# Optimization experiments

Measured on AMD Instinct MI355X. Metric: run time of the kernel, lower is better.

The kernel has to match this reference:

```python
import jax, jax.numpy as jnp
import numpy as np

E = 1024
H = 16
DH = E // H
LN_EPS = 1e-5


def setup_inputs() -> dict:
    key = jax.random.key(0)
    ks = jax.random.split(key, 9)
    B, Lq, Lk = 8, 1024, 1024
    s = 0.02
    return {
        "query": jax.random.normal(ks[0], (B, Lq, E), jnp.float32),
        "key_t": jax.random.normal(ks[1], (B, Lk, E), jnp.float32),
        "value": jax.random.normal(ks[2], (B, Lk, E), jnp.float32),
        "in_proj_w": jax.random.normal(ks[3], (3 * E, E), jnp.float32) * s,
        "in_proj_b": jnp.zeros((3 * E,), jnp.float32),
        "out_proj_w": jax.random.normal(ks[4], (E, E), jnp.float32) * s,
        "out_proj_b": jnp.zeros((E,), jnp.float32),
        "ln_gamma": jnp.ones((E,), jnp.float32),
        "ln_beta": jnp.zeros((E,), jnp.float32),
    }


def _mha_cross(query, key_t, value, in_proj_w, in_proj_b, out_proj_w, out_proj_b,
               ln_gamma, ln_beta):
    B, Lq, _ = query.shape
    Lk = key_t.shape[1]
    wq, wk, wv = in_proj_w[:E], in_proj_w[E:2 * E], in_proj_w[2 * E:]
    bq, bk, bv = in_proj_b[:E], in_proj_b[E:2 * E], in_proj_b[2 * E:]
    # projections (torch Linear: x @ W^T + b)
    q = (query @ wq.T + bq).reshape(B, Lq, H, DH)
    k = (key_t @ wk.T + bk).reshape(B, Lk, H, DH)
    v = (value @ wv.T + bv).reshape(B, Lk, H, DH)
    scale = 1.0 / np.sqrt(DH).astype(np.float32)
    # unfused attention: explicit [B,H,Lq,Lk] scores (need_weights=True path)
    scores = jnp.einsum("bqhd,bkhd->bhqk", q, k) * scale
    probs = jax.nn.softmax(scores, axis=-1)
    attn = jnp.einsum("bhqk,bkhd->bqhd", probs, v).reshape(B, Lq, E)
    attn_out = attn @ out_proj_w.T + out_proj_b
    # averaged attention weights (average_attn_weights=True default)
    attn_weights = probs.mean(axis=1)  # [B, Lq, Lk]
    # residual + LayerNorm
    x = query + attn_out
    mu = x.mean(axis=-1, keepdims=True)
    var = x.var(axis=-1, keepdims=True)
    y = (x - mu) * jax.lax.rsqrt(var + LN_EPS) * ln_gamma + ln_beta
    return y, attn_weights


def reference(query, key_t, value, in_proj_w, in_proj_b, out_proj_w, out_proj_b,
              ln_gamma, ln_beta):
    return _mha_cross(query, key_t, value, in_proj_w, in_proj_b,
                      out_proj_w, out_proj_b, ln_gamma, ln_beta)
```

## Files before the change

kernel.cpp:

```cpp
#include <hip/hip_runtime.h>
#include <stdint.h>

#define E_DIM 1024
#define H_NUM 16
#define B_NUM 8
#define LQ 1024
#define LK 1024
#define MROWS (B_NUM * LQ)

typedef unsigned short u16;
typedef __attribute__((ext_vector_type(8))) short bf16x8;
typedef __attribute__((ext_vector_type(4))) short bf16x4;
typedef __attribute__((ext_vector_type(4))) float f32x4;
typedef bf16x8 __attribute__((may_alias)) bf16x8_ma;
typedef bf16x4 __attribute__((may_alias)) bf16x4_ma;
typedef f32x4 __attribute__((may_alias)) f32x4_ma;

typedef __attribute__((address_space(1))) const void* gas_ptr;
typedef __attribute__((address_space(3))) void* las_ptr;

__device__ __forceinline__ void gload16(const void* g, void* l) {
  __builtin_amdgcn_global_load_lds((gas_ptr)g, (las_ptr)l, 16, 0, 0);
}

__device__ __forceinline__ u16 f2bf(float f) {
  union { float f; uint32_t u; } c; c.f = f;
  return (u16)((c.u + 0x7FFFu + ((c.u >> 16) & 1u)) >> 16);
}

#define MFMA_BF16(a, b, c) __builtin_amdgcn_mfma_f32_16x16x32_bf16((a), (b), (c), 0, 0, 0)

#define SCALE_Q 0.18033688011112042f

__global__ __launch_bounds__(256) void cvt_f32_bf16(const float* __restrict__ src,
                                                    u16* __restrict__ dst, int n4) {
  int i = blockIdx.x * 256 + threadIdx.x;
  const int stride = gridDim.x * 256;
  for (; i < n4; i += stride) {
    float4 v = ((const float4*)src)[i];
    ushort4 o;
    o.x = f2bf(v.x); o.y = f2bf(v.y); o.z = f2bf(v.z); o.w = f2bf(v.w);
    ((ushort4*)dst)[i] = o;
  }
}

__global__ __launch_bounds__(256) void cvt3_f32_bf16(
    const float* __restrict__ a0, const float* __restrict__ a1, const float* __restrict__ a2,
    u16* __restrict__ o0, u16* __restrict__ o1, u16* __restrict__ o2, int n4) {
  const float* s = (blockIdx.y == 0) ? a0 : (blockIdx.y == 1 ? a1 : a2);
  u16* d = (blockIdx.y == 0) ? o0 : (blockIdx.y == 1 ? o1 : o2);
  int i = blockIdx.x * 256 + threadIdx.x;
  const int stride = gridDim.x * 256;
  for (; i < n4; i += stride) {
    float4 v = ((const float4*)s)[i];
    ushort4 o;
    o.x = f2bf(v.x); o.y = f2bf(v.y); o.z = f2bf(v.z); o.w = f2bf(v.w);
    ((ushort4*)d)[i] = o;
  }
}


#define BAR() __builtin_amdgcn_s_barrier()
#define LGKM0() do { asm volatile("s_waitcnt lgkmcnt(0)" ::: "memory"); \
                     __builtin_amdgcn_sched_barrier(0); } while (0)
#define LGKM8() asm volatile("s_waitcnt lgkmcnt(8)" ::: "memory")
#define VMC(n) asm volatile("s_waitcnt vmcnt(" n ")" ::: "memory")

#define STAGEH(mat, rowbase, kt, ldsoff)                                     \
  { const u16* _s = (mat) + (size_t)(rowbase) * E_DIM + (kt);                \
    gload16(_s + goff0, ldsv + (ldsoff) + wave * 1024);                      \
    gload16(_s + goff1, ldsv + (ldsoff) + 8192 + wave * 1024); }

#define READ_B(db)                                                           \
  _Pragma("unroll") for (int n = 0; n < 4; ++n) {                            \
    const int rgb = wn4 + n;                                                 \
    _Pragma("unroll") for (int ks = 0; ks < 2; ++ks)                         \
      bfr[n][ks] = *(const bf16x8_ma*)(ldsc + 65536 + (db) * 32768 +         \
          ((rgb >> 3) << 14) + (((rgb & 7) * 2 + ks) << 10) + lanebase);     \
  }

#define READ_A(db, q)                                                        \
  _Pragma("unroll") for (int jj = 0; jj < 2; ++jj) {                         \
    const int rga = 4 * (q) + 2 * jj + wm;                                   \
    _Pragma("unroll") for (int ks = 0; ks < 2; ++ks)                         \
      afr[jj][ks] = *(const bf16x8_ma*)(ldsc + (db) * 32768 +                \
          ((rga >> 3) << 14) + (((rga & 7) * 2 + ks) << 10) + lanebase);     \
  }

#define MMA(q)                                                               \
  __builtin_amdgcn_s_setprio(1);                                             \
  _Pragma("unroll") for (int jj = 0; jj < 2; ++jj)                           \
    _Pragma("unroll") for (int n = 0; n < 4; ++n)                            \
      _Pragma("unroll") for (int ks = 0; ks < 2; ++ks)                       \
        acc[2 * (q) + jj][n] =                                               \
            MFMA_BF16(afr[jj][ks], bfr[n][ks], acc[2 * (q) + jj][n]);        \
  __builtin_amdgcn_s_setprio(0);

template <int MODE>
__global__ __launch_bounds__(512, 2) void gemm256(
    const u16* __restrict__ A0, const u16* __restrict__ A1, const u16* __restrict__ A2,
    const u16* __restrict__ W, const float* __restrict__ bias,
    const float* __restrict__ resid,
    u16* __restrict__ outb, float* __restrict__ outf,
    int nwg_n, int nwg_m) {
  __shared__ u16 lds[65536];

  const int tid = threadIdx.x;
  const int wave = tid >> 6, lane = tid & 63;
  const int lr = lane & 15, lg = lane >> 4;
  const int wm = wave >> 2, wn4 = (wave & 3) * 4;

  const int cpx = (int)gridDim.x >> 3;
  const int bid = blockIdx.x;
  const int wg = (bid & 7) * cpx + (bid >> 3);
  const int n_i = wg % nwg_n;
  const int rest = wg / nwg_n;
  const int m_i = rest % nwg_m;
  const int z = rest / nwg_m;
  const int m0 = m_i * 256, n0 = n_i * 256;

  const u16* Az = (z == 0) ? A0 : (z == 1 ? A1 : A2);
  const u16* Wz = W + (size_t)z * E_DIM * E_DIM;
  const float* bs = bias + z * E_DIM;
  const float scale = (MODE == 0 && z == 0) ? SCALE_Q : 1.0f;

  int goff0, goff1;
  {
    const int X0 = wave * 1024 + lane * 16;
    const int L0 = X0 ^ (((X0 >> 9) & 1) << 5);
    goff0 = (((L0 >> 10) >> 1) * 16 + ((L0 >> 6) & 15)) * E_DIM +
            ((L0 >> 10) & 1) * 32 + ((L0 & 63) >> 1);
    const int X1 = 8192 + X0;
    const int L1 = X1 ^ (((X1 >> 9) & 1) << 5);
    goff1 = (((L1 >> 10) >> 1) * 16 + ((L1 >> 6) & 15)) * E_DIM +
            ((L1 >> 10) & 1) * 32 + ((L1 & 63) >> 1);
  }
  const char* ldsc = (const char*)lds;
  char* ldsv = (char*)lds;
  const int lanebase = lr * 64 + ((lg * 16) ^ ((lane & 8) << 2));

  const f32x4 fzero = {0.f, 0.f, 0.f, 0.f};
  f32x4 acc[8][4];
#pragma unroll
  for (int j = 0; j < 8; ++j)
#pragma unroll
    for (int n = 0; n < 4; ++n) acc[j][n] = fzero;

  STAGEH(Az, m0,       0,  0);
  STAGEH(Az, m0 + 128, 0,  16384);
  STAGEH(Wz, n0,       0,  65536);
  STAGEH(Wz, n0 + 128, 0,  65536 + 16384);
  STAGEH(Wz, n0,       64, 65536 + 32768);
  STAGEH(Wz, n0 + 128, 64, 65536 + 32768 + 16384);
  STAGEH(Az, m0,       64, 32768);
  VMC("6");
  BAR();

  bf16x8 bfr[4][2], afr[2][2];
#pragma unroll 1
  for (int i = 0; i < 8; ++i) {
    const int kt2 = i * 128 + 128;
    const bool nl = (i < 7);
    READ_B(0) READ_A(0, 0)
    STAGEH(Az, m0 + 128, i * 128 + 64, 32768 + 16384);
    LGKM8();
    BAR(); LGKM0();
    MMA(0)
    BAR();
    READ_A(0, 1)
    if (nl) STAGEH(Wz, n0, kt2, 65536);
    BAR(); LGKM0();
    MMA(1)
    BAR();
    READ_A(0, 2)
    if (nl) STAGEH(Az, m0, kt2, 0);
    BAR(); LGKM0();
    MMA(2)
    BAR();
    READ_A(0, 3)
    if (nl) {
      STAGEH(Wz, n0 + 128, kt2, 65536 + 16384);
      VMC("6");
    } else {
      VMC("0");
    }
    BAR(); LGKM0();
    MMA(3)
    BAR();
    READ_B(1) READ_A(1, 0)
    if (nl) STAGEH(Az, m0 + 128, kt2, 16384);
    LGKM8();
    BAR(); LGKM0();
    MMA(0)
    BAR();
    READ_A(1, 1)
    if (nl) STAGEH(Wz, n0, kt2 + 64, 65536 + 32768);
    BAR(); LGKM0();
    MMA(1)
    BAR();
    READ_A(1, 2)
    if (nl) STAGEH(Wz, n0 + 128, kt2 + 64, 65536 + 32768 + 16384);
    BAR(); LGKM0();
    MMA(2)
    BAR();
    READ_A(1, 3)
    if (nl) {
      STAGEH(Az, m0, kt2 + 64, 32768);
      VMC("6");
    }
    BAR(); LGKM0();
    MMA(3)
    BAR();
  }

  float bvv[4];
#pragma unroll
  for (int n = 0; n < 4; ++n) bvv[n] = bs[n0 + wn4 * 16 + n * 16 + lr];

  if (MODE == 0) {
    u16* Cb = outb + (size_t)z * (size_t)MROWS * E_DIM;
#pragma unroll
    for (int j = 0; j < 8; ++j) {
      const int rbase = m0 + (2 * j + wm) * 16 + lg * 4;
#pragma unroll
      for (int ii = 0; ii < 4; ++ii) {
        const size_t m = (size_t)(rbase + ii);
#pragma unroll
        for (int n = 0; n < 4; ++n) {
          const int nn = n0 + wn4 * 16 + n * 16 + lr;
          Cb[m * E_DIM + nn] = f2bf((acc[j][n][ii] + bvv[n]) * scale);
        }
      }
    }
  } else {
#pragma unroll
    for (int j = 0; j < 8; ++j) {
      const int rbase = m0 + (2 * j + wm) * 16 + lg * 4;
#pragma unroll
      for (int ii = 0; ii < 4; ++ii) {
        const size_t m = (size_t)(rbase + ii);
#pragma unroll
        for (int n = 0; n < 4; ++n) {
          const int nn = n0 + wn4 * 16 + n * 16 + lr;
          outf[m * E_DIM + nn] = acc[j][n][ii] + bvv[n] + resid[m * E_DIM + nn];
        }
      }
    }
  }
}

__global__ __launch_bounds__(256) void gemm128_out(
    const u16* __restrict__ A, const u16* __restrict__ W,
    const float* __restrict__ bias, const float* __restrict__ resid,
    float* __restrict__ outf, int nwg_n, int nwg_m) {
  __shared__ u16 As[128 * 64];
  __shared__ u16 Bs[128 * 64];

  const int tid = threadIdx.x;
  const int wave = tid >> 6;
  const int lane = tid & 63;
  const int lr = lane & 15, lg = lane >> 4;
  const int wr = wave >> 1, wc = wave & 1;

  const int cpx = (int)gridDim.x >> 3;
  const int bid = blockIdx.x;
  const int wg = (bid & 7) * cpx + (bid >> 3);
  const int n_i = wg % nwg_n;
  const int m_i = (wg / nwg_n) % nwg_m;

  const int m0 = m_i * 128;
  const int n0 = n_i * 128;

  const f32x4 fzero = {0.f, 0.f, 0.f, 0.f};
  f32x4 acc[4][4];
#pragma unroll
  for (int a = 0; a < 4; ++a)
#pragma unroll
    for (int b = 0; b < 4; ++b) acc[a][b] = fzero;

  const int lrow8 = lane >> 3;
  const int lcol8 = (lane & 7) * 8;

  for (int kt = 0; kt < E_DIM; kt += 64) {
#pragma unroll
    for (int i = 0; i < 4; ++i) {
      const int seg = i * 4 + wave;
      gload16(W + (size_t)(n0 + seg * 8 + lrow8) * E_DIM + kt + lcol8, &Bs[seg * 512]);
      gload16(A + (size_t)(m0 + seg * 8 + lrow8) * E_DIM + kt + lcol8, &As[seg * 512]);
    }
    __syncthreads();

#pragma unroll
    for (int kk = 0; kk < 64; kk += 32) {
      bf16x8 av[4], bv[4];
#pragma unroll
      for (int t = 0; t < 4; ++t)
        av[t] = *(const bf16x8*)&As[(wr * 64 + t * 16 + lr) * 64 + kk + lg * 8];
#pragma unroll
      for (int t = 0; t < 4; ++t)
        bv[t] = *(const bf16x8*)&Bs[(wc * 64 + t * 16 + lr) * 64 + kk + lg * 8];
#pragma unroll
      for (int mi = 0; mi < 4; ++mi)
#pragma unroll
        for (int ni = 0; ni < 4; ++ni)
          acc[mi][ni] = MFMA_BF16(av[mi], bv[ni], acc[mi][ni]);
    }
    __syncthreads();
  }

  float bvv[4];
#pragma unroll
  for (int ni = 0; ni < 4; ++ni) bvv[ni] = bias[n0 + wc * 64 + ni * 16 + lr];

#pragma unroll
  for (int mi = 0; mi < 4; ++mi) {
#pragma unroll
    for (int i = 0; i < 4; ++i) {
      const size_t m = (size_t)(m0 + wr * 64 + mi * 16 + lg * 4 + i);
#pragma unroll
      for (int ni = 0; ni < 4; ++ni) {
        const int n = n0 + wc * 64 + ni * 16 + lr;
        outf[m * E_DIM + n] = acc[mi][ni][i] + bvv[ni] + resid[m * E_DIM + n];
      }
    }
  }
}

__global__ __launch_bounds__(256) void transpose_v(const u16* __restrict__ Vb,
                                                   u16* __restrict__ Vtg) {
  __shared__ u16 T[64 * 264];
  const int tid = threadIdx.x;
  const int b = blockIdx.z, h = blockIdx.y;
  const int k0 = blockIdx.x * 256;
  const int bh = b * H_NUM + h;
  const int krow = tid >> 3;
  const int d0 = (tid & 7) * 8;
  const int jst = krow & 7;
#pragma unroll
  for (int it = 0; it < 8; ++it) {
    const int k = it * 32 + krow;
    bf16x8 v = *(const bf16x8*)&Vb[(size_t)(b * LK + k0 + k) * E_DIM + h * 64 + d0];
#pragma unroll
    for (int jj = 0; jj < 8; ++jj) {
      const int j = (jj + jst) & 7;
      T[(d0 + j) * 264 + k] = (u16)v[j];
    }
  }
  __syncthreads();
  const int d = tid >> 2;
  const int kk0 = (tid & 3) * 64;
  u16* orow = &Vtg[(size_t)(bh * 64 + d) * LK + k0 + kk0];
#pragma unroll
  for (int c = 0; c < 8; ++c)
    *(bf16x8*)&orow[c * 8] = *(const bf16x8*)&T[d * 264 + kk0 + c * 8];
}

__global__ __launch_bounds__(256) void attn_fwd(
    const u16* __restrict__ Qb, const u16* __restrict__ Kb, const u16* __restrict__ Vtg,
    u16* __restrict__ attnb, float* __restrict__ rden) {
  __shared__ u16 Ks[64 * 72];
  __shared__ u16 Vt[64 * 72];
  __shared__ u16 Pw[4][16 * 72];

  const int tid = threadIdx.x;
  const int wave = tid >> 6, lane = tid & 63;
  const int lr = lane & 15, lg = lane >> 4;

  const int bid = blockIdx.x;
  const int wg = (bid & 7) * 256 + (bid >> 3);
  const int qt = wg & 15;
  const int h = (wg >> 4) & 15;
  const int b = wg >> 8;
  const int bh = b * H_NUM + h;
  const int q0 = qt * 64;

  const size_t qoff = (size_t)(b * LQ + q0 + wave * 16 + lr) * E_DIM + h * 64;
  const bf16x8 qf0 = *(const bf16x8*)&Qb[qoff + lg * 8];
  const bf16x8 qf1 = *(const bf16x8*)&Qb[qoff + 32 + lg * 8];

  const f32x4 fzero = {0.f, 0.f, 0.f, 0.f};
  f32x4 ctx[4];
#pragma unroll
  for (int d = 0; d < 4; ++d) ctx[d] = fzero;
  float dnl = 0.f;

  const int sr = tid >> 2;
  const int sc = (tid & 3) * 16;
  const u16* Kg = &Kb[(size_t)(b * LK + sr) * E_DIM + h * 64 + sc];
  const u16* Vg = &Vtg[(size_t)(bh * 64 + sr) * LK + sc];

  bf16x8 kr0 = *(const bf16x8*)(Kg);
  bf16x8 kr1 = *(const bf16x8*)(Kg + 8);
  bf16x8 vr0 = *(const bf16x8*)(Vg);
  bf16x8 vr1 = *(const bf16x8*)(Vg + 8);
  *(bf16x8*)&Ks[sr * 72 + sc] = kr0; *(bf16x8*)&Ks[sr * 72 + sc + 8] = kr1;
  *(bf16x8*)&Vt[sr * 72 + sc] = vr0; *(bf16x8*)&Vt[sr * 72 + sc + 8] = vr1;

  for (int t = 0; t < 16; ++t) {
    __syncthreads();
    if (t < 15) {
      const int k1 = (t + 1) * 64;
      kr0 = *(const bf16x8*)(Kg + (size_t)k1 * E_DIM);
      kr1 = *(const bf16x8*)(Kg + (size_t)k1 * E_DIM + 8);
      vr0 = *(const bf16x8*)(Vg + k1);
      vr1 = *(const bf16x8*)(Vg + k1 + 8);
    }
#pragma unroll
    for (int kf = 0; kf < 4; ++kf) {
      const bf16x8 kb0 = *(const bf16x8*)&Ks[(kf * 16 + lr) * 72 + lg * 8];
      const bf16x8 kb1 = *(const bf16x8*)&Ks[(kf * 16 + lr) * 72 + 32 + lg * 8];
      f32x4 s = fzero;
      s = MFMA_BF16(kb0, qf0, s);
      s = MFMA_BF16(kb1, qf1, s);
      const float p0 = exp2f(s[0]), p1 = exp2f(s[1]);
      const float p2 = exp2f(s[2]), p3 = exp2f(s[3]);
      dnl += (p0 + p1) + (p2 + p3);
      bf16x4 w;
      w[0] = (short)f2bf(p0); w[1] = (short)f2bf(p1);
      w[2] = (short)f2bf(p2); w[3] = (short)f2bf(p3);
      *(bf16x4_ma*)&Pw[wave][lr * 72 + kf * 16 + lg * 4] = w;
    }
    const bf16x8 pa0 = *(const bf16x8_ma*)&Pw[wave][lr * 72 + lg * 8];
    const bf16x8 pa1 = *(const bf16x8_ma*)&Pw[wave][lr * 72 + 32 + lg * 8];
#pragma unroll
    for (int df = 0; df < 4; ++df) {
      const bf16x8 vb0 = *(const bf16x8*)&Vt[(df * 16 + lr) * 72 + lg * 8];
      const bf16x8 vb1 = *(const bf16x8*)&Vt[(df * 16 + lr) * 72 + 32 + lg * 8];
      ctx[df] = MFMA_BF16(pa0, vb0, ctx[df]);
      ctx[df] = MFMA_BF16(pa1, vb1, ctx[df]);
    }
    __syncthreads();
    if (t < 15) {
      *(bf16x8*)&Ks[sr * 72 + sc] = kr0; *(bf16x8*)&Ks[sr * 72 + sc + 8] = kr1;
      *(bf16x8*)&Vt[sr * 72 + sc] = vr0; *(bf16x8*)&Vt[sr * 72 + sc + 8] = vr1;
    }
  }

  dnl += __shfl_xor(dnl, 16, 64);
  dnl += __shfl_xor(dnl, 32, 64);
  if (lane < 16) rden[(size_t)bh * LQ + q0 + wave * 16 + lane] = 0.0625f / dnl;
  float dnv[4];
#pragma unroll
  for (int i = 0; i < 4; ++i) dnv[i] = __shfl(dnl, lg * 4 + i, 64);

#pragma unroll
  for (int i = 0; i < 4; ++i) {
    const float inv = 1.0f / dnv[i];
    const int q = q0 + wave * 16 + lg * 4 + i;
    const size_t orow = (size_t)(b * LQ + q) * E_DIM + h * 64;
#pragma unroll
    for (int df = 0; df < 4; ++df)
      attnb[orow + df * 16 + lr] = f2bf(ctx[df][i] * inv);
  }
}

__global__ __launch_bounds__(256) void attn_wts(
    const u16* __restrict__ Qb, const u16* __restrict__ Kb,
    const float* __restrict__ rden, float* __restrict__ aw) {
  __shared__ u16 Ks2[2][128 * 72];

  const int tid = threadIdx.x;
  const int wave = tid >> 6, lane = tid & 63;
  const int lr = lane & 15, lg = lane >> 4;

  const int bid = blockIdx.x;
  const int wg = (bid & 7) * 128 + (bid >> 3);
  const int q0 = (wg & 15) * 64;
  const int k0 = ((wg >> 4) & 7) * 128;
  const int b = wg >> 7;

  const f32x4 fzero = {0.f, 0.f, 0.f, 0.f};
  f32x4 acc[2][4];
#pragma unroll
  for (int t = 0; t < 2; ++t)
#pragma unroll
    for (int f = 0; f < 4; ++f) acc[t][f] = fzero;

  const int sr = tid >> 1;
  const int sc = (tid & 1) * 32;
  const u16* Kg = &Kb[(size_t)(b * LK + k0 + sr) * E_DIM + sc];
  const size_t qbase = (size_t)(b * LQ + q0 + lr) * E_DIM;
  const size_t dbase = (size_t)(b * H_NUM) * LQ + q0 + lr;

  {
    bf16x8 r0 = *(const bf16x8*)(Kg);
    bf16x8 r1 = *(const bf16x8*)(Kg + 8);
    bf16x8 r2 = *(const bf16x8*)(Kg + 16);
    bf16x8 r3 = *(const bf16x8*)(Kg + 24);
    *(bf16x8*)&Ks2[0][sr * 72 + sc] = r0;      *(bf16x8*)&Ks2[0][sr * 72 + sc + 8] = r1;
    *(bf16x8*)&Ks2[0][sr * 72 + sc + 16] = r2; *(bf16x8*)&Ks2[0][sr * 72 + sc + 24] = r3;
  }

  for (int h = 0; h < H_NUM; ++h) {
    bf16x8 r0, r1, r2, r3;
    if (h < 15) {
      const u16* Kn = Kg + (h + 1) * 64;
      r0 = *(const bf16x8*)(Kn);
      r1 = *(const bf16x8*)(Kn + 8);
      r2 = *(const bf16x8*)(Kn + 16);
      r3 = *(const bf16x8*)(Kn + 24);
    }
    float rd[4];
#pragma unroll
    for (int j = 0; j < 4; ++j) rd[j] = rden[dbase + (size_t)h * LQ + j * 16];

    __syncthreads();

    const u16* Kbuf = &Ks2[h & 1][0];
#pragma unroll
    for (int j = 0; j < 4; ++j) {
      const bf16x8 qf0 = *(const bf16x8*)&Qb[qbase + (size_t)(j * 16) * E_DIM + h * 64 + lg * 8];
      const bf16x8 qf1 = *(const bf16x8*)&Qb[qbase + (size_t)(j * 16) * E_DIM + h * 64 + 32 + lg * 8];
#pragma unroll
      for (int t = 0; t < 2; ++t) {
        const int row = wave * 32 + t * 16 + lr;
        const bf16x8 kb0 = *(const bf16x8*)&Kbuf[row * 72 + lg * 8];
        const bf16x8 kb1 = *(const bf16x8*)&Kbuf[row * 72 + 32 + lg * 8];
        f32x4 s = fzero;
        s = MFMA_BF16(kb0, qf0, s);
        s = MFMA_BF16(kb1, qf1, s);
#pragma unroll
        for (int i = 0; i < 4; ++i)
          acc[t][j][i] += __builtin_amdgcn_exp2f(s[i]) * rd[j];
      }
    }

    if (h < 15) {
      u16* Kw = &Ks2[(h + 1) & 1][0];
      *(bf16x8*)&Kw[sr * 72 + sc] = r0;      *(bf16x8*)&Kw[sr * 72 + sc + 8] = r1;
      *(bf16x8*)&Kw[sr * 72 + sc + 16] = r2; *(bf16x8*)&Kw[sr * 72 + sc + 24] = r3;
    }
  }

#pragma unroll
  for (int j = 0; j < 4; ++j) {
    const size_t orow = (size_t)(b * LQ + q0 + j * 16 + lr) * LK;
#pragma unroll
    for (int t = 0; t < 2; ++t)
      *(f32x4_ma*)&aw[orow + k0 + wave * 32 + t * 16 + lg * 4] = acc[t][j];
  }
}

__global__ __launch_bounds__(256) void ln_kernel(float* __restrict__ xy,
                                                 const float* __restrict__ gamma,
                                                 const float* __restrict__ beta) {
  __shared__ float ls[4], ls2[4];
  const int row = blockIdx.x;
  const int tid = threadIdx.x;
  float4* xr = (float4*)(xy + (size_t)row * E_DIM);
  float4 v = xr[tid];
  float s = v.x + v.y + v.z + v.w;
  float s2 = v.x * v.x + v.y * v.y + v.z * v.z + v.w * v.w;
#pragma unroll
  for (int off = 32; off >= 1; off >>= 1) {
    s += __shfl_xor(s, off, 64);
    s2 += __shfl_xor(s2, off, 64);
  }
  const int wave = tid >> 6, lane = tid & 63;
  if (lane == 0) { ls[wave] = s; ls2[wave] = s2; }
  __syncthreads();
  s = ls[0] + ls[1] + ls[2] + ls[3];
  s2 = ls2[0] + ls2[1] + ls2[2] + ls2[3];
  const float mu = s * (1.0f / E_DIM);
  const float var = s2 * (1.0f / E_DIM) - mu * mu;
  const float rs = rsqrtf(var + 1e-5f);
  const float4 g = ((const float4*)gamma)[tid];
  const float4 bt = ((const float4*)beta)[tid];
  float4 o;
  o.x = (v.x - mu) * rs * g.x + bt.x;
  o.y = (v.y - mu) * rs * g.y + bt.y;
  o.z = (v.z - mu) * rs * g.z + bt.z;
  o.w = (v.w - mu) * rs * g.w + bt.w;
  xr[tid] = o;
}

extern "C" void kernel_launch(void* const* d_in, const int* in_sizes, int n_in,
                              void* d_out, int out_size, void* d_ws, size_t ws_size,
                              hipStream_t stream) {
  (void)in_sizes; (void)n_in; (void)out_size; (void)ws_size;
  const float* query     = (const float*)d_in[0];
  const float* key_t     = (const float*)d_in[1];
  const float* value     = (const float*)d_in[2];
  const float* in_proj_b = (const float*)d_in[4];
  const float* out_proj_b = (const float*)d_in[6];
  const float* ln_gamma  = (const float*)d_in[7];
  const float* ln_beta   = (const float*)d_in[8];

  float* y  = (float*)d_out;
  float* aw = y + (size_t)B_NUM * LQ * E_DIM;

  const size_t SZ = (size_t)B_NUM * LQ * E_DIM;
  u16* ws    = (u16*)d_ws;
  u16* Qb    = ws;
  u16* Kb    = ws + SZ;
  u16* Vb    = ws + 2 * SZ;
  u16* attnb = ws + 3 * SZ;
  u16* wqkvb = ws + 4 * SZ;
  u16* woutb = wqkvb + 3 * E_DIM * E_DIM;
  float* rden = (float*)(wqkvb + 4 * (size_t)E_DIM * E_DIM);

  u16* Xq  = (u16*)aw;
  u16* Xk  = Xq + SZ;
  u16* Xv  = (u16*)y;
  u16* Vtg = (u16*)y;

  cvt_f32_bf16<<<3072, 256, 0, stream>>>((const float*)d_in[3], wqkvb, (3 * E_DIM * E_DIM) / 4);
  cvt_f32_bf16<<<1024, 256, 0, stream>>>((const float*)d_in[5], woutb, (E_DIM * E_DIM) / 4);
  cvt3_f32_bf16<<<dim3(2048, 3), 256, 0, stream>>>(query, key_t, value, Xq, Xk, Xv, (int)(SZ / 4));

  gemm256<0><<<384, 512, 0, stream>>>(
      Xq, Xk, Xv, wqkvb, in_proj_b, nullptr, Qb, nullptr, 4, 32);

  transpose_v<<<dim3(4, 16, 8), 256, 0, stream>>>(Vb, Vtg);

  attn_fwd<<<2048, 256, 0, stream>>>(Qb, Kb, Vtg, attnb, rden);

  attn_wts<<<1024, 256, 0, stream>>>(Qb, Kb, rden, aw);

  gemm128_out<<<512, 256, 0, stream>>>(attnb, woutb, out_proj_b, query, y, 8, 64);

  ln_kernel<<<8192, 256, 0, stream>>>(y, ln_gamma, ln_beta);
}
```

Measured before the change: 300.0 us.

## Enlarge attn_wts tile to 128x128 and stage Q through shared memory

The attention-weights kernel now covers 128 query rows by 128 key rows per block, with a 2x2 wave layout in which each wave computes a 64x64 sub-tile. Q is prefetched into registers and staged through LDS each head instead of being loaded directly from global memory by every wave, and K fragments are hoisted into registers for reuse across four query sub-tiles. The goal is to halve K reloads per output and cut redundant global Q traffic. The cost is an extra barrier per head, more LDS, and more accumulator registers (launch bounds now 256,2). The exp intrinsic also changes from __builtin_amdgcn_exp2f to exp2f, which may compile to slower code.

After: 272.5 us. 1.1x faster.

```diff
diff --git a/kernel.cpp b/kernel.cpp
--- a/kernel.cpp
+++ b/kernel.cpp
@@ -454,90 +454,97 @@
   }
 }
 
-__global__ __launch_bounds__(256) void attn_wts(
+__global__ __launch_bounds__(256, 2) void attn_wts(
     const u16* __restrict__ Qb, const u16* __restrict__ Kb,
     const float* __restrict__ rden, float* __restrict__ aw) {
   __shared__ u16 Ks2[2][128 * 72];
+  __shared__ u16 Qs[128 * 72];
 
   const int tid = threadIdx.x;
   const int wave = tid >> 6, lane = tid & 63;
   const int lr = lane & 15, lg = lane >> 4;
+  const int wq = wave >> 1, wk = wave & 1;
 
   const int bid = blockIdx.x;
-  const int wg = (bid & 7) * 128 + (bid >> 3);
-  const int q0 = (wg & 15) * 64;
-  const int k0 = ((wg >> 4) & 7) * 128;
-  const int b = wg >> 7;
+  const int wg = (bid & 7) * 64 + (bid >> 3);
+  const int q0 = (wg & 7) * 128;
+  const int k0 = ((wg >> 3) & 7) * 128;
+  const int b = wg >> 6;
 
   const f32x4 fzero = {0.f, 0.f, 0.f, 0.f};
-  f32x4 acc[2][4];
-#pragma unroll
-  for (int t = 0; t < 2; ++t)
-#pragma unroll
-    for (int f = 0; f < 4; ++f) acc[t][f] = fzero;
+  f32x4 acc[4][4];
+#pragma unroll
+  for (int t = 0; t < 4; ++t)
+#pragma unroll
+    for (int j = 0; j < 4; ++j) acc[t][j] = fzero;
 
   const int sr = tid >> 1;
   const int sc = (tid & 1) * 32;
   const u16* Kg = &Kb[(size_t)(b * LK + k0 + sr) * E_DIM + sc];
-  const size_t qbase = (size_t)(b * LQ + q0 + lr) * E_DIM;
-  const size_t dbase = (size_t)(b * H_NUM) * LQ + q0 + lr;
-
-  {
-    bf16x8 r0 = *(const bf16x8*)(Kg);
-    bf16x8 r1 = *(const bf16x8*)(Kg + 8);
-    bf16x8 r2 = *(const bf16x8*)(Kg + 16);
-    bf16x8 r3 = *(const bf16x8*)(Kg + 24);
-    *(bf16x8*)&Ks2[0][sr * 72 + sc] = r0;      *(bf16x8*)&Ks2[0][sr * 72 + sc + 8] = r1;
-    *(bf16x8*)&Ks2[0][sr * 72 + sc + 16] = r2; *(bf16x8*)&Ks2[0][sr * 72 + sc + 24] = r3;
-  }
+  const u16* Qg = &Qb[(size_t)(b * LQ + q0 + sr) * E_DIM + sc];
+  const float* dg = &rden[(size_t)(b * H_NUM) * LQ + q0 + wq * 64 + lr];
+
+  bf16x8 kr[4], qr[4];
+#pragma unroll
+  for (int c = 0; c < 4; ++c) kr[c] = *(const bf16x8*)(Kg + c * 8);
+#pragma unroll
+  for (int c = 0; c < 4; ++c) qr[c] = *(const bf16x8*)(Qg + c * 8);
+#pragma unroll
+  for (int c = 0; c < 4; ++c) *(bf16x8*)&Ks2[0][sr * 72 + sc + c * 8] = kr[c];
 
   for (int h = 0; h < H_NUM; ++h) {
-    bf16x8 r0, r1, r2, r3;
+    __syncthreads();
+#pragma unroll
+    for (int c = 0; c < 4; ++c) *(bf16x8*)&Qs[sr * 72 + sc + c * 8] = qr[c];
+    __syncthreads();
+
     if (h < 15) {
-      const u16* Kn = Kg + (h + 1) * 64;
-      r0 = *(const bf16x8*)(Kn);
-      r1 = *(const bf16x8*)(Kn + 8);
-      r2 = *(const bf16x8*)(Kn + 16);
-      r3 = *(const bf16x8*)(Kn + 24);
+#pragma unroll
+      for (int c = 0; c < 4; ++c) kr[c] = *(const bf16x8*)(Kg + (h + 1) * 64 + c * 8);
+#pragma unroll
+      for (int c = 0; c < 4; ++c) qr[c] = *(const bf16x8*)(Qg + (h + 1) * 64 + c * 8);
     }
     float rd[4];
 #pragma unroll
-    for (int j = 0; j < 4; ++j) rd[j] = rden[dbase + (size_t)h * LQ + j * 16];
-
-    __syncthreads();
+    for (int j = 0; j < 4; ++j) rd[j] = dg[(size_t)h * LQ + j * 16];
 
     const u16* Kbuf = &Ks2[h & 1][0];
+    bf16x8 kb[4][2];
+#pragma unroll
+    for (int t = 0; t < 4; ++t) {
+      const int row = wk * 64 + t * 16 + lr;
+      kb[t][0] = *(const bf16x8*)&Kbuf[row * 72 + lg * 8];
+      kb[t][1] = *(const bf16x8*)&Kbuf[row * 72 + 32 + lg * 8];
+    }
 #pragma unroll
     for (int j = 0; j < 4; ++j) {
-      const bf16x8 qf0 = *(const bf16x8*)&Qb[qbase + (size_t)(j * 16) * E_DIM + h * 64 + lg * 8];
-      const bf16x8 qf1 = *(const bf16x8*)&Qb[qbase + (size_t)(j * 16) * E_DIM + h * 64 + 32 + lg * 8];
-#pragma unroll
-      for (int t = 0; t < 2; ++t) {
-        const int row = wave * 32 + t * 16 + lr;
-        const bf16x8 kb0 = *(const bf16x8*)&Kbuf[row * 72 + lg * 8];
-        const bf16x8 kb1 = *(const bf16x8*)&Kbuf[row * 72 + 32 + lg * 8];
+      const int qrow = wq * 64 + j * 16 + lr;
+      const bf16x8 qf0 = *(const bf16x8*)&Qs[qrow * 72 + lg * 8];
+      const bf16x8 qf1 = *(const bf16x8*)&Qs[qrow * 72 + 32 + lg * 8];
+#pragma unroll
+      for (int t = 0; t < 4; ++t) {
         f32x4 s = fzero;
-        s = MFMA_BF16(kb0, qf0, s);
-        s = MFMA_BF16(kb1, qf1, s);
+        s = MFMA_BF16(kb[t][0], qf0, s);
+        s = MFMA_BF16(kb[t][1], qf1, s);
 #pragma unroll
         for (int i = 0; i < 4; ++i)
-          acc[t][j][i] += __builtin_amdgcn_exp2f(s[i]) * rd[j];
+          acc[t][j][i] += exp2f(s[i]) * rd[j];
       }
     }
 
     if (h < 15) {
       u16* Kw = &Ks2[(h + 1) & 1][0];
-      *(bf16x8*)&Kw[sr * 72 + sc] = r0;      *(bf16x8*)&Kw[sr * 72 + sc + 8] = r1;
-      *(bf16x8*)&Kw[sr * 72 + sc + 16] = r2; *(bf16x8*)&Kw[sr * 72 + sc + 24] = r3;
+#pragma unroll
+      for (int c = 0; c < 4; ++c) *(bf16x8*)&Kw[sr * 72 + sc + c * 8] = kr[c];
     }
   }
 
 #pragma unroll
   for (int j = 0; j < 4; ++j) {
-    const size_t orow = (size_t)(b * LQ + q0 + j * 16 + lr) * LK;
-#pragma unroll
-    for (int t = 0; t < 2; ++t)
-      *(f32x4_ma*)&aw[orow + k0 + wave * 32 + t * 16 + lg * 4] = acc[t][j];
+    const size_t orow = (size_t)(b * LQ + q0 + wq * 64 + j * 16 + lr) * LK;
+#pragma unroll
+    for (int t = 0; t < 4; ++t)
+      *(f32x4_ma*)&aw[orow + k0 + wk * 64 + t * 16 + lg * 4] = acc[t][j];
   }
 }
 
@@ -615,7 +622,7 @@
 
   attn_fwd<<<2048, 256, 0, stream>>>(Qb, Kb, Vtg, attnb, rden);
 
-  attn_wts<<<1024, 256, 0, stream>>>(Qb, Kb, rden, aw);
+  attn_wts<<<512, 256, 0, stream>>>(Qb, Kb, rden, aw);
 
   gemm128_out<<<512, 256, 0, stream>>>(attnb, woutb, out_proj_b, query, y, 8, 64);
 
```
